# Performance work log

Hardware: AMD Instinct MI355X
Metric: run time of the kernel (lower is better)

## Reference

```python
import jax, jax.numpy as jnp
import numpy as np

D_MODEL = 1024
N_HEADS = 16
D_K = D_MODEL // N_HEADS


def setup_inputs() -> dict:
    key = jax.random.key(0)
    k1, k2, k3 = jax.random.split(key, 3)
    x = jax.random.normal(k1, (4, 2048, D_MODEL), dtype=jnp.float32)
    # torch Linear weight shape (out, in); y = x @ W.T
    w_qkv = jax.random.normal(k2, (3 * D_MODEL, D_MODEL), dtype=jnp.float32) * (1.0 / np.sqrt(D_MODEL))
    w_o = jax.random.normal(k3, (D_MODEL, D_MODEL), dtype=jnp.float32) * (1.0 / np.sqrt(D_MODEL))
    return {"x": x, "w_qkv": w_qkv, "w_o": w_o}


def reference(x, w_qkv, w_o):
    B, T, C = x.shape
    qkv = jnp.einsum('btc,fc->btf', x, w_qkv)              # [B,T,3C]
    qkv = qkv.reshape(B, T, 3, N_HEADS, D_K).transpose(2, 0, 3, 1, 4)  # [3,B,H,T,dk]
    q, k, v = qkv[0], qkv[1], qkv[2]
    scale = 1.0 / np.sqrt(D_K).astype(np.float32)
    attn = jnp.einsum('bhqd,bhkd->bhqk', q, k) * scale     # [B,H,T,T]
    attn = jax.nn.softmax(attn, axis=-1)
    out = jnp.einsum('bhqk,bhkd->bhqd', attn, v)           # [B,H,T,dk]
    out = out.transpose(0, 2, 1, 3).reshape(B, T, C)
    return jnp.einsum('btc,oc->bto', out, w_o)
```

## Files before the change

### kernel.cpp

```cpp
#include <hip/hip_runtime.h>
#include <hip/hip_bf16.h>
#include <stdint.h>


#define B_   4
#define T_   2048
#define H_   16
#define DK_  64
#define C_   1024
#define M_   (B_*T_)
#define N1_  (3*C_)
#define LOG2E 1.44269504088896340736f
#define SCFOLD (0.125f * LOG2E)

using short8  = __attribute__((ext_vector_type(8))) short;
using short4v = __attribute__((ext_vector_type(4))) short;
using f32x4   = __attribute__((ext_vector_type(4))) float;
typedef unsigned short u16;

__device__ __forceinline__ u16 f2bf(float f) {
  unsigned u = __float_as_uint(f);
  u += 0x7FFF + ((u >> 16) & 1);
  return (u16)(u >> 16);
}

__device__ __forceinline__ short4v packexp(f32x4 s) {
  unsigned u0 = __float_as_uint(__builtin_amdgcn_exp2f(s[0]));
  unsigned u1 = __float_as_uint(__builtin_amdgcn_exp2f(s[1]));
  unsigned u2 = __float_as_uint(__builtin_amdgcn_exp2f(s[2]));
  unsigned u3 = __float_as_uint(__builtin_amdgcn_exp2f(s[3]));
  union { unsigned w[2]; short4v s4; } cv;
  cv.w[0] = __builtin_amdgcn_perm(u1, u0, 0x07060302);
  cv.w[1] = __builtin_amdgcn_perm(u3, u2, 0x07060302);
  return cv.s4;
}

__device__ __forceinline__ void gld_lds16(void* lds, const void* g) {
  __builtin_amdgcn_global_load_lds(
      (__attribute__((address_space(1))) void*)(g),
      (__attribute__((address_space(3))) void*)(lds), 16, 0, 0);
}

__global__ void cast_all(const float* __restrict__ x, const float* __restrict__ wq,
                         const float* __restrict__ wo, u16* __restrict__ xb,
                         u16* __restrict__ wqb, u16* __restrict__ wob) {
  const int nx = M_ * C_ / 4, nq = N1_ * C_ / 4;
  int i = blockIdx.x * blockDim.x + threadIdx.x;
  const float* src; u16* dst; int j;
  if (i < nx)            { src = x;  dst = xb;  j = i; }
  else if (i < nx + nq)  { src = wq; dst = wqb; j = i - nx; }
  else                   { src = wo; dst = wob; j = i - nx - nq; }
  float4 v = ((const float4*)src)[j];
  ushort4 o;
  o.x = f2bf(v.x); o.y = f2bf(v.y); o.z = f2bf(v.z); o.w = f2bf(v.w);
  ((ushort4*)dst)[j] = o;
}

template <int MODE>
__global__ __launch_bounds__(256)
void gemm_bt(const u16* __restrict__ A, const u16* __restrict__ Bm,
             void* __restrict__ out0, void* __restrict__ out1, void* __restrict__ out2,
             int K, int N) {
  __shared__ __attribute__((aligned(16))) u16 As[128 * 32];
  __shared__ __attribute__((aligned(16))) u16 Bs[128 * 32];
  const int tid  = threadIdx.x;
  const int w    = tid >> 6, lane = tid & 63;
  const int quad = lane >> 4, l15 = lane & 15;
  const int wm   = w >> 1, wn = w & 1;
  const int m0   = blockIdx.y * 128, n0 = blockIdx.x * 128;

  f32x4 acc[4][4];
#pragma unroll
  for (int i = 0; i < 4; i++)
#pragma unroll
    for (int j = 0; j < 4; j++) acc[i][j] = f32x4{0.f, 0.f, 0.f, 0.f};

  const int nkt = K >> 5;
  for (int kt = 0; kt < nkt; ++kt) {
    __syncthreads();
#pragma unroll
    for (int c = 0; c < 2; ++c) {
      int chunk = c * 256 + tid;
      int row = chunk >> 2, col = (chunk & 3) << 3;
      gld_lds16(As + (c * 256 + w * 64) * 8, A  + (size_t)(m0 + row) * K + kt * 32 + col);
      gld_lds16(Bs + (c * 256 + w * 64) * 8, Bm + (size_t)(n0 + row) * K + kt * 32 + col);
    }
    __syncthreads();
    short8 af[4], bf[4];
#pragma unroll
    for (int i = 0; i < 4; i++)
      af[i] = *(const short8*)(As + (wm * 64 + i * 16 + l15) * 32 + quad * 8);
#pragma unroll
    for (int j = 0; j < 4; j++)
      bf[j] = *(const short8*)(Bs + (wn * 64 + j * 16 + l15) * 32 + quad * 8);
#pragma unroll
    for (int i = 0; i < 4; i++)
#pragma unroll
      for (int j = 0; j < 4; j++)
        acc[i][j] = __builtin_amdgcn_mfma_f32_16x16x32_bf16(af[i], bf[j], acc[i][j], 0, 0, 0);
  }

  if (MODE == 0) {
    u16* q  = (u16*)out0;
    u16* k  = (u16*)out1;
    u16* vt = (u16*)out2;
#pragma unroll
    for (int i = 0; i < 4; i++) {
      int m = m0 + wm * 64 + i * 16 + quad * 4;
      int b = m >> 11, t = m & 2047;
#pragma unroll
      for (int j = 0; j < 4; j++) {
        int f = n0 + wn * 64 + j * 16 + l15;
        int s = f >> 10, h = (f >> 6) & 15, d = f & 63;
        if (s == 2) {
          ushort4 pk;
          pk.x = f2bf(acc[i][j][0]); pk.y = f2bf(acc[i][j][1]);
          pk.z = f2bf(acc[i][j][2]); pk.w = f2bf(acc[i][j][3]);
          int kt2 = t >> 6;
          int u   = (t >> 2) & 15;
          int pp  = u ^ (d & 15);
          *(ushort4*)(vt + ((((size_t)(b * H_ + h) * 32 + kt2) * 64 + d) * 16 + pp) * 4) = pk;
        } else {
          u16* dst = (s == 0) ? q : k;
          float sc = (s == 0) ? SCFOLD : 1.0f;
#pragma unroll
          for (int r = 0; r < 4; r++)
            dst[(((size_t)(b * H_ + h)) * T_ + (t + r)) * DK_ + d] = f2bf(acc[i][j][r] * sc);
        }
      }
    }
  } else {
    float* outp = (float*)out0;
#pragma unroll
    for (int i = 0; i < 4; i++) {
      int m = m0 + wm * 64 + i * 16 + quad * 4;
#pragma unroll
      for (int j = 0; j < 4; j++) {
        int n = n0 + wn * 64 + j * 16 + l15;
#pragma unroll
        for (int r = 0; r < 4; r++)
          outp[(size_t)(m + r) * N + n] = acc[i][j][r];
      }
    }
  }
}

__global__ __launch_bounds__(256)
void flash_kernel(const u16* __restrict__ Q, const u16* __restrict__ Kg,
                  const u16* __restrict__ Vt, u16* __restrict__ AO) {
  __shared__ __attribute__((aligned(16))) u16 KVs[2][2][64 * 64];
  const int tid  = threadIdx.x;
  const int w    = tid >> 6, lane = tid & 63;
  const int quad = lane >> 4, l15 = lane & 15;
  const int bh   = blockIdx.x;
  const int q0   = blockIdx.y * 128;
  const u16* Qb = Q  + (size_t)bh * T_ * DK_;
  const u16* Kb = Kg + (size_t)bh * T_ * DK_;
  const u16* Vb = Vt + (size_t)bh * T_ * DK_;

  short8 qf[2][2];
#pragma unroll
  for (int mi = 0; mi < 2; mi++)
#pragma unroll
    for (int ks = 0; ks < 2; ks++)
      qf[mi][ks] = *(const short8*)(Qb + (size_t)(q0 + w * 32 + mi * 16 + l15) * DK_ + ks * 32 + quad * 8);

  short4v ones;
#pragma unroll
  for (int z = 0; z < 4; z++) ones[z] = (short)0x3F80;

  f32x4 O[2][4];
  f32x4 rowsum[2];
#pragma unroll
  for (int mi = 0; mi < 2; mi++) {
    rowsum[mi] = f32x4{0.f, 0.f, 0.f, 0.f};
#pragma unroll
    for (int dj = 0; dj < 4; dj++) O[mi][dj] = f32x4{0.f, 0.f, 0.f, 0.f};
  }

  const int swz = l15 & 7;
  const int NT  = T_ / 64;
  const int koff0 = ((quad) ^ swz) * 8;
  const int koff1 = ((4 + quad) ^ swz) * 8;
  int voff[4];
#pragma unroll
  for (int nj = 0; nj < 4; nj++) voff[nj] = ((nj * 4 + quad) ^ l15) * 4;

  auto stage = [&](int kt, int b) {
#pragma unroll
    for (int c = 0; c < 2; ++c) {
      int s = c * 256 + tid;
      int row = s >> 3, cc = (s & 7) ^ (row & 7);
      gld_lds16(&KVs[b][0][(c * 256 + w * 64) * 8], Kb + (size_t)kt * 4096 + row * 64 + cc * 8);
      gld_lds16(&KVs[b][1][(c * 256 + w * 64) * 8], Vb + (size_t)kt * 4096 + s * 8);
    }
  };

  stage(0, 0);

  for (int kt = 0; kt < NT; ++kt) {
    __syncthreads();
    if (kt + 1 < NT) stage(kt + 1, (kt + 1) & 1);
    const u16* Ks = KVs[kt & 1][0];
    const u16* Vs = KVs[kt & 1][1];

    f32x4 stc0, stc1, stn0, stn1;
    {
      const u16* krow = Ks + l15 * 64;
      short8 kfr0 = *(const short8*)(krow + koff0);
      short8 kfr1 = *(const short8*)(krow + koff1);
      stc0 = f32x4{0.f, 0.f, 0.f, 0.f};
      stc1 = f32x4{0.f, 0.f, 0.f, 0.f};
      stc0 = __builtin_amdgcn_mfma_f32_16x16x32_bf16(kfr0, qf[0][0], stc0, 0, 0, 0);
      stc0 = __builtin_amdgcn_mfma_f32_16x16x32_bf16(kfr1, qf[0][1], stc0, 0, 0, 0);
      stc1 = __builtin_amdgcn_mfma_f32_16x16x32_bf16(kfr0, qf[1][0], stc1, 0, 0, 0);
      stc1 = __builtin_amdgcn_mfma_f32_16x16x32_bf16(kfr1, qf[1][1], stc1, 0, 0, 0);
    }
#pragma unroll
    for (int nj = 0; nj < 4; nj++) {
      if (nj < 3) {
        const u16* krow = Ks + ((nj + 1) * 16 + l15) * 64;
        short8 kfr0 = *(const short8*)(krow + koff0);
        short8 kfr1 = *(const short8*)(krow + koff1);
        stn0 = f32x4{0.f, 0.f, 0.f, 0.f};
        stn1 = f32x4{0.f, 0.f, 0.f, 0.f};
        stn0 = __builtin_amdgcn_mfma_f32_16x16x32_bf16(kfr0, qf[0][0], stn0, 0, 0, 0);
        stn0 = __builtin_amdgcn_mfma_f32_16x16x32_bf16(kfr1, qf[0][1], stn0, 0, 0, 0);
        stn1 = __builtin_amdgcn_mfma_f32_16x16x32_bf16(kfr0, qf[1][0], stn1, 0, 0, 0);
        stn1 = __builtin_amdgcn_mfma_f32_16x16x32_bf16(kfr1, qf[1][1], stn1, 0, 0, 0);
      }
      short4v pf0 = packexp(stc0);
      short4v pf1 = packexp(stc1);
      rowsum[0] = __builtin_amdgcn_mfma_f32_16x16x16bf16_1k(pf0, ones, rowsum[0], 0, 0, 0);
      rowsum[1] = __builtin_amdgcn_mfma_f32_16x16x16bf16_1k(pf1, ones, rowsum[1], 0, 0, 0);
#pragma unroll
      for (int dj = 0; dj < 4; dj++) {
        short4v vfr = *(const short4v*)(Vs + (dj * 16 + l15) * 64 + voff[nj]);
        O[0][dj] = __builtin_amdgcn_mfma_f32_16x16x16bf16_1k(pf0, vfr, O[0][dj], 0, 0, 0);
        O[1][dj] = __builtin_amdgcn_mfma_f32_16x16x16bf16_1k(pf1, vfr, O[1][dj], 0, 0, 0);
      }
      stc0 = stn0;
      stc1 = stn1;
    }
  }

  const int b = bh >> 4, h = bh & 15;
#pragma unroll
  for (int mi = 0; mi < 2; mi++) {
#pragma unroll
    for (int r = 0; r < 4; r++) {
      float inv = 1.0f / rowsum[mi][r];
      int t = q0 + w * 32 + mi * 16 + quad * 4 + r;
#pragma unroll
      for (int dj = 0; dj < 4; dj++)
        AO[((size_t)(b * T_ + t)) * C_ + h * DK_ + dj * 16 + l15] = f2bf(O[mi][dj][r] * inv);
    }
  }
}

extern "C" void kernel_launch(void* const* d_in, const int* in_sizes, int n_in,
                              void* d_out, int out_size, void* d_ws, size_t ws_size,
                              hipStream_t stream) {
  const float* x    = (const float*)d_in[0];
  const float* wqkv = (const float*)d_in[1];
  const float* wo   = (const float*)d_in[2];

  char* p = (char*)d_ws;
  u16* xb    = (u16*)p; p += (size_t)M_ * C_ * 2;
  u16* wqkvb = (u16*)p; p += (size_t)N1_ * C_ * 2;
  u16* wob   = (u16*)p; p += (size_t)C_ * C_ * 2;
  u16* qb    = (u16*)p; p += (size_t)M_ * C_ * 2;
  u16* kb    = (u16*)p; p += (size_t)M_ * C_ * 2;
  u16* vtb   = (u16*)p; p += (size_t)M_ * C_ * 2;
  u16* aob   = (u16*)p; p += (size_t)M_ * C_ * 2;

  const int ncast = (M_ * C_ + N1_ * C_ + C_ * C_) / 4;
  cast_all<<<(ncast + 255) / 256, 256, 0, stream>>>(x, wqkv, wo, xb, wqkvb, wob);

  gemm_bt<0><<<dim3(N1_ / 128, M_ / 128), 256, 0, stream>>>(xb, wqkvb, qb, kb, vtb, C_, N1_);

  flash_kernel<<<dim3(B_ * H_, T_ / 128), 256, 0, stream>>>(qb, kb, vtb, aob);

  gemm_bt<1><<<dim3(C_ / 128, M_ / 128), 256, 0, stream>>>(aob, wob, d_out, nullptr, nullptr, C_, C_);
}
```

Measured before the change: 284.9 us.

## Use 16x16x32 bf16 MFMA for PV and rowsum with remapped K rows and V layout

After: 274.0 us. 3.8% less time.

```diff
diff --git a/kernel.cpp b/kernel.cpp
--- a/kernel.cpp
+++ b/kernel.cpp
@@ -33,6 +33,10 @@
   cv.w[0] = __builtin_amdgcn_perm(u1, u0, 0x07060302);
   cv.w[1] = __builtin_amdgcn_perm(u3, u2, 0x07060302);
   return cv.s4;
+}
+
+__device__ __forceinline__ short8 cat44(short4v a, short4v b) {
+  return __builtin_shufflevector(a, b, 0, 1, 2, 3, 4, 5, 6, 7);
 }
 
 __device__ __forceinline__ void gld_lds16(void* lds, const void* g) {
@@ -116,10 +120,11 @@
           ushort4 pk;
           pk.x = f2bf(acc[i][j][0]); pk.y = f2bf(acc[i][j][1]);
           pk.z = f2bf(acc[i][j][2]); pk.w = f2bf(acc[i][j][3]);
-          int kt2 = t >> 6;
-          int u   = (t >> 2) & 15;
-          int pp  = u ^ (d & 15);
-          *(ushort4*)(vt + ((((size_t)(b * H_ + h) * 32 + kt2) * 64 + d) * 16 + pp) * 4) = pk;
+          int kt2  = t >> 6;
+          int cw   = (t >> 3) & 7;
+          int pw   = cw ^ (d & 7);
+          int half = (t >> 2) & 1;
+          *(ushort4*)(vt + ((((size_t)(b * H_ + h) * 32 + kt2) * 64 + d) * 8 + pw) * 8 + half * 4) = pk;
         } else {
           u16* dst = (s == 0) ? q : k;
           float sc = (s == 0) ? SCFOLD : 1.0f;
@@ -165,9 +170,9 @@
     for (int ks = 0; ks < 2; ks++)
       qf[mi][ks] = *(const short8*)(Qb + (size_t)(q0 + w * 32 + mi * 16 + l15) * DK_ + ks * 32 + quad * 8);
 
-  short4v ones;
-#pragma unroll
-  for (int z = 0; z < 4; z++) ones[z] = (short)0x3F80;
+  short8 ones8;
+#pragma unroll
+  for (int z = 0; z < 8; z++) ones8[z] = (short)0x3F80;
 
   f32x4 O[2][4];
   f32x4 rowsum[2];
@@ -182,15 +187,14 @@
   const int NT  = T_ / 64;
   const int koff0 = ((quad) ^ swz) * 8;
   const int koff1 = ((4 + quad) ^ swz) * 8;
-  int voff[4];
-#pragma unroll
-  for (int nj = 0; nj < 4; nj++) voff[nj] = ((nj * 4 + quad) ^ l15) * 4;
+  const int rA    = ((l15 >> 2) << 3) + (l15 & 3);
 
   auto stage = [&](int kt, int b) {
 #pragma unroll
     for (int c = 0; c < 2; ++c) {
       int s = c * 256 + tid;
-      int row = s >> 3, cc = (s & 7) ^ (row & 7);
+      int row = s >> 3;
+      int cc  = (s & 7) ^ ((row & 3) | (((row >> 3) & 1) << 2));
       gld_lds16(&KVs[b][0][(c * 256 + w * 64) * 8], Kb + (size_t)kt * 4096 + row * 64 + cc * 8);
       gld_lds16(&KVs[b][1][(c * 256 + w * 64) * 8], Vb + (size_t)kt * 4096 + s * 8);
     }
@@ -204,43 +208,54 @@
     const u16* Ks = KVs[kt & 1][0];
     const u16* Vs = KVs[kt & 1][1];
 
-    f32x4 stc0, stc1, stn0, stn1;
+    f32x4 sA0c, sA1c, sB0c, sB1c, sA0n, sA1n, sB0n, sB1n;
     {
-      const u16* krow = Ks + l15 * 64;
-      short8 kfr0 = *(const short8*)(krow + koff0);
-      short8 kfr1 = *(const short8*)(krow + koff1);
-      stc0 = f32x4{0.f, 0.f, 0.f, 0.f};
-      stc1 = f32x4{0.f, 0.f, 0.f, 0.f};
-      stc0 = __builtin_amdgcn_mfma_f32_16x16x32_bf16(kfr0, qf[0][0], stc0, 0, 0, 0);
-      stc0 = __builtin_amdgcn_mfma_f32_16x16x32_bf16(kfr1, qf[0][1], stc0, 0, 0, 0);
-      stc1 = __builtin_amdgcn_mfma_f32_16x16x32_bf16(kfr0, qf[1][0], stc1, 0, 0, 0);
-      stc1 = __builtin_amdgcn_mfma_f32_16x16x32_bf16(kfr1, qf[1][1], stc1, 0, 0, 0);
-    }
-#pragma unroll
-    for (int nj = 0; nj < 4; nj++) {
-      if (nj < 3) {
-        const u16* krow = Ks + ((nj + 1) * 16 + l15) * 64;
-        short8 kfr0 = *(const short8*)(krow + koff0);
-        short8 kfr1 = *(const short8*)(krow + koff1);
-        stn0 = f32x4{0.f, 0.f, 0.f, 0.f};
-        stn1 = f32x4{0.f, 0.f, 0.f, 0.f};
-        stn0 = __builtin_amdgcn_mfma_f32_16x16x32_bf16(kfr0, qf[0][0], stn0, 0, 0, 0);
-        stn0 = __builtin_amdgcn_mfma_f32_16x16x32_bf16(kfr1, qf[0][1], stn0, 0, 0, 0);
-        stn1 = __builtin_amdgcn_mfma_f32_16x16x32_bf16(kfr0, qf[1][0], stn1, 0, 0, 0);
-        stn1 = __builtin_amdgcn_mfma_f32_16x16x32_bf16(kfr1, qf[1][1], stn1, 0, 0, 0);
+      const u16* krA = Ks + (rA)     * 64;
+      const u16* krB = Ks + (rA + 4) * 64;
+      short8 ka0 = *(const short8*)(krA + koff0);
+      short8 ka1 = *(const short8*)(krA + koff1);
+      short8 kb0 = *(const short8*)(krB + koff0);
+      short8 kb1 = *(const short8*)(krB + koff1);
+      sA0c = f32x4{0.f, 0.f, 0.f, 0.f}; sA1c = sA0c; sB0c = sA0c; sB1c = sA0c;
+      sA0c = __builtin_amdgcn_mfma_f32_16x16x32_bf16(ka0, qf[0][0], sA0c, 0, 0, 0);
+      sA0c = __builtin_amdgcn_mfma_f32_16x16x32_bf16(ka1, qf[0][1], sA0c, 0, 0, 0);
+      sA1c = __builtin_amdgcn_mfma_f32_16x16x32_bf16(ka0, qf[1][0], sA1c, 0, 0, 0);
+      sA1c = __builtin_amdgcn_mfma_f32_16x16x32_bf16(ka1, qf[1][1], sA1c, 0, 0, 0);
+      sB0c = __builtin_amdgcn_mfma_f32_16x16x32_bf16(kb0, qf[0][0], sB0c, 0, 0, 0);
+      sB0c = __builtin_amdgcn_mfma_f32_16x16x32_bf16(kb1, qf[0][1], sB0c, 0, 0, 0);
+      sB1c = __builtin_amdgcn_mfma_f32_16x16x32_bf16(kb0, qf[1][0], sB1c, 0, 0, 0);
+      sB1c = __builtin_amdgcn_mfma_f32_16x16x32_bf16(kb1, qf[1][1], sB1c, 0, 0, 0);
+    }
+#pragma unroll
+    for (int u = 0; u < 2; ++u) {
+      if (u == 0) {
+        const u16* krA = Ks + (32 + rA)     * 64;
+        const u16* krB = Ks + (32 + rA + 4) * 64;
+        short8 ka0 = *(const short8*)(krA + koff0);
+        short8 ka1 = *(const short8*)(krA + koff1);
+        short8 kb0 = *(const short8*)(krB + koff0);
+        short8 kb1 = *(const short8*)(krB + koff1);
+        sA0n = f32x4{0.f, 0.f, 0.f, 0.f}; sA1n = sA0n; sB0n = sA0n; sB1n = sA0n;
+        sA0n = __builtin_amdgcn_mfma_f32_16x16x32_bf16(ka0, qf[0][0], sA0n, 0, 0, 0);
+        sA0n = __builtin_amdgcn_mfma_f32_16x16x32_bf16(ka1, qf[0][1], sA0n, 0, 0, 0);
+        sA1n = __builtin_amdgcn_mfma_f32_16x16x32_bf16(ka0, qf[1][0], sA1n, 0, 0, 0);
+        sA1n = __builtin_amdgcn_mfma_f32_16x16x32_bf16(ka1, qf[1][1], sA1n, 0, 0, 0);
+        sB0n = __builtin_amdgcn_mfma_f32_16x16x32_bf16(kb0, qf[0][0], sB0n, 0, 0, 0);
+        sB0n = __builtin_amdgcn_mfma_f32_16x16x32_bf16(kb1, qf[0][1], sB0n, 0, 0, 0);
+        sB1n = __builtin_amdgcn_mfma_f32_16x16x32_bf16(kb0, qf[1][0], sB1n, 0, 0, 0);
+        sB1n = __builtin_amdgcn_mfma_f32_16x16x32_bf16(kb1, qf[1][1], sB1n, 0, 0, 0);
       }
-      short4v pf0 = packexp(stc0);
-      short4v pf1 = packexp(stc1);
-      rowsum[0] = __builtin_amdgcn_mfma_f32_16x16x16bf16_1k(pf0, ones, rowsum[0], 0, 0, 0);
-      rowsum[1] = __builtin_amdgcn_mfma_f32_16x16x16bf16_1k(pf1, ones, rowsum[1], 0, 0, 0);
+      short8 pa0 = cat44(packexp(sA0c), packexp(sB0c));
+      short8 pa1 = cat44(packexp(sA1c), packexp(sB1c));
+      rowsum[0] = __builtin_amdgcn_mfma_f32_16x16x32_bf16(pa0, ones8, rowsum[0], 0, 0, 0);
+      rowsum[1] = __builtin_amdgcn_mfma_f32_16x16x32_bf16(pa1, ones8, rowsum[1], 0, 0, 0);
 #pragma unroll
       for (int dj = 0; dj < 4; dj++) {
-        short4v vfr = *(const short4v*)(Vs + (dj * 16 + l15) * 64 + voff[nj]);
-        O[0][dj] = __builtin_amdgcn_mfma_f32_16x16x16bf16_1k(pf0, vfr, O[0][dj], 0, 0, 0);
-        O[1][dj] = __builtin_amdgcn_mfma_f32_16x16x16bf16_1k(pf1, vfr, O[1][dj], 0, 0, 0);
+        short8 vfr = *(const short8*)(Vs + (dj * 16 + l15) * 64 + ((4 * u + quad) ^ swz) * 8);
+        O[0][dj] = __builtin_amdgcn_mfma_f32_16x16x32_bf16(pa0, vfr, O[0][dj], 0, 0, 0);
+        O[1][dj] = __builtin_amdgcn_mfma_f32_16x16x32_bf16(pa1, vfr, O[1][dj], 0, 0, 0);
       }
-      stc0 = stn0;
-      stc1 = stn1;
+      sA0c = sA0n; sA1c = sA1n; sB0c = sB0n; sB1c = sB1n;
     }
   }
 
```
